# Kernel optimization log

Hardware: AMD Instinct MI355X
Metric: run time of the kernel (lower is better)

Reference implementation:

```python
import jax, jax.numpy as jnp
import numpy as np
from math import sqrt

N_USERS = 60000
N_ITEMS = 40000
D = 64
B = 3
LAYERS = 2
E = 600000
BATCH = 2048
N_NODES = (N_USERS + 1) + (N_ITEMS + 1)
REG_WEIGHT = 1e-3
BPR_GAMMA = 1e-10


def setup_inputs() -> dict:
    key = jax.random.key(0)
    k0, k1, k2, k3, k4 = jax.random.split(key, 5)
    user_emb = jax.random.normal(k0, (N_USERS + 1, D), jnp.float32) * 0.1
    item_emb = jax.random.normal(k1, (N_ITEMS + 1, D), jnp.float32) * 0.1
    W = jnp.ones((B,), jnp.float32)
    edge_users = jax.random.randint(k2, (B, E), 1, N_USERS + 1)
    edge_items = jax.random.randint(k3, (B, E), 1, N_ITEMS + 1)
    batch_data = jax.random.randint(k4, (BATCH, B, 3), 1, N_ITEMS + 1)
    return dict(user_emb=user_emb, item_emb=item_emb, W=W,
                edge_users=edge_users, edge_items=edge_items,
                batch_data=batch_data)


def _lightgcn(emb, eu, ei, layers):
    # bipartite undirected graph: users <-> items (items offset by N_USERS+1)
    it = ei + (N_USERS + 1)
    src = jnp.concatenate([eu, it])
    dst = jnp.concatenate([it, eu])
    deg = jax.ops.segment_sum(jnp.ones_like(src, jnp.float32), src, N_NODES)
    norm = jax.lax.rsqrt(jnp.maximum(deg[src], 1.0)) * jax.lax.rsqrt(jnp.maximum(deg[dst], 1.0))
    out = emb
    cur = emb
    for _ in range(layers):
        cur = jax.ops.segment_sum(cur[src] * norm[:, None], dst, N_NODES)
        out = out + cur
    return out / (layers + 1)


def _mutual_attention(f):
    # f: [N, B, D]
    S = jnp.einsum('nid,njd->nij', f, f)          # [N, B, B] pairwise scores
    last = S[:, B - 1:B, :]                        # [N, 1, B]
    proj = S[:, :B - 1, :]                         # [N, B-1, B]
    # (last * proj) * last / (last^2 + eps)   (dim-1 is size 1, sums/norms trivial)
    clear = (last * proj) * last / (last * last + 1e-12)   # [N, B-1, B]
    scores = jnp.sum(clear, axis=1, keepdims=True) + last   # [N, 1, B]
    all_scores = jnp.concatenate([clear, scores], axis=1)   # [N, B, B]
    att = jax.nn.softmax(all_scores / sqrt(D), axis=-1)
    return jnp.einsum('nij,njd->nid', att, f)


def reference(user_emb, item_emb, W, edge_users, edge_items, batch_data):
    total0 = jnp.concatenate([user_emb, item_emb], axis=0)   # [N_NODES, D]
    # global graph = union of all behaviors
    g_eu = edge_users.reshape(-1)
    g_ei = edge_items.reshape(-1)
    all_emb = _lightgcn(total0, g_eu, g_ei, LAYERS)
    # per-behavior propagation
    u_list, i_list = [], []
    for b in range(B):
        eb = _lightgcn(all_emb, edge_users[b], edge_items[b], LAYERS)
        u_list.append(eb[:N_USERS + 1])
        i_list.append(eb[N_USERS + 1:])
    all_user = jnp.stack(u_list, axis=1)   # [n_users+1, B, D]
    all_item = jnp.stack(i_list, axis=1)   # [n_items+1, B, D]
    all_user = _mutual_attention(all_user)
    # item behaviour degree: interactions per item per behavior
    ones = jnp.ones((E,), jnp.float32)
    ibd = jnp.stack([jax.ops.segment_sum(ones, edge_items[b], N_ITEMS + 1)
                     for b in range(B)], axis=1)   # [n_items+1, B]
    weight = ibd * W
    weight = weight / (jnp.sum(weight, axis=1, keepdims=True) + 1e-8)
    item_final = jnp.sum(all_item * weight[:, :, None], axis=1)   # [n_items+1, D]
    total_loss = jnp.float32(0.0)
    for b in range(B):
        users = batch_data[:, b, 0]
        items = batch_data[:, b, 1:3]
        uf = all_user[:, b][users][:, None, :]      # [batch, 1, D]
        itf = item_final[items]                      # [batch, 2, D]
        scores = jnp.sum(uf * itf, axis=2)           # [batch, 2]
        total_loss = total_loss - jnp.mean(
            jnp.log(BPR_GAMMA + jax.nn.sigmoid(scores[:, 0] - scores[:, 1])))
    emb_loss = (jnp.linalg.norm(user_emb) + jnp.linalg.norm(item_emb)) / (N_ITEMS + 1)
    return total_loss + REG_WEIGHT * emb_loss
```

## Files before the change

kernel.cpp:

```cpp
#include <hip/hip_runtime.h>
#include <hip/hip_bf16.h>
#include <math.h>

#define NUQ 60001
#define NIQ 40001
#define NNQ 100002
#define DQ  64
#define EQ  600000
#define BQ  3
#define BATCHQ 2048
#define ROWW 32
#define NSLOT (BATCHQ * BQ)
#define NPAD 100004
#define ADJB 1200000
#define BLK_ELE 2048
#define NBLK ((NNQ + BLK_ELE - 1) / BLK_ELE)
#define RANGE 392
#define NRANGE 256
#define NBINS (BQ * NRANGE)
#define NBLKA 256
#define EPB ((BQ * EQ + NBLKA - 1) / NBLKA)

__device__ __forceinline__ float wave_sum(float v) {
#pragma unroll
  for (int m = 32; m >= 1; m >>= 1) v += __shfl_xor(v, m, 64);
  return v;
}
__device__ __forceinline__ int wave_sum_i(int v) {
#pragma unroll
  for (int m = 32; m >= 1; m >>= 1) v += __shfl_xor(v, m, 64);
  return v;
}

__device__ __forceinline__ unsigned pack_bf2(float lo, float hi) {
  unsigned a = __float_as_uint(lo);
  unsigned b = __float_as_uint(hi);
  a = (a + 0x7FFFu + ((a >> 16) & 1u)) >> 16;
  b = (b + 0x7FFFu + ((b >> 16) & 1u)) >> 16;
  return a | (b << 16);
}
__device__ __forceinline__ float unpk_lo(unsigned u) { return __uint_as_float(u << 16); }
__device__ __forceinline__ float unpk_hi(unsigned u) { return __uint_as_float(u & 0xFFFF0000u); }

__device__ __forceinline__ void ntst_u32(unsigned* p, unsigned v) { __builtin_nontemporal_store(v, p); }
__device__ __forceinline__ void ntst_f32(float* p, float v) { __builtin_nontemporal_store(v, p); }
__device__ __forceinline__ unsigned ntld_u32(const unsigned* p) { return __builtin_nontemporal_load(p); }
__device__ __forceinline__ float ntld_f32(const float* p) { return __builtin_nontemporal_load(p); }

__global__ void zero_i_k(int* __restrict__ p, int n) {
  int tid = blockIdx.x * blockDim.x + threadIdx.x;
  int stride = gridDim.x * blockDim.x;
  for (int i = tid; i < n; i += stride) p[i] = 0;
}

__global__ void sumsq_k(const float* __restrict__ p, int n, float* __restrict__ acc) {
  int tid = blockIdx.x * blockDim.x + threadIdx.x;
  int stride = gridDim.x * blockDim.x;
  float s = 0.f;
  for (int i = tid; i < n; i += stride) { float v = p[i]; s += v * v; }
  s = wave_sum(s);
  __shared__ float ws[4];
  if ((threadIdx.x & 63) == 0) ws[threadIdx.x >> 6] = s;
  __syncthreads();
  if (threadIdx.x == 0) atomicAdd(acc, ws[0] + ws[1] + ws[2] + ws[3]);
}

__global__ void binc_k(const int* __restrict__ eu, const int* __restrict__ ei,
                       unsigned* __restrict__ counts) {
  __shared__ unsigned h[NBINS];
  for (int i = threadIdx.x; i < NBINS; i += 256) h[i] = 0u;
  __syncthreads();
  int base = blockIdx.x * EPB;
  int end = base + EPB;
  if (end > BQ * EQ) end = BQ * EQ;
  for (int idx = base + threadIdx.x; idx < end; idx += 256) {
    int b = idx / EQ;
    int u = eu[idx];
    int it = ei[idx] + NUQ;
    atomicAdd(&h[b * NRANGE + u / RANGE], 1u);
    atomicAdd(&h[b * NRANGE + it / RANGE], 1u);
  }
  __syncthreads();
  for (int i = threadIdx.x; i < NBINS; i += 256)
    counts[(size_t)blockIdx.x * NBINS + i] = h[i];
}

__global__ void binscan1_k(const unsigned* __restrict__ counts,
                           unsigned* __restrict__ offs, unsigned* __restrict__ bintot) {
  int bin = blockIdx.x;
  int t = threadIdx.x;
  int lane = t & 63, wid = t >> 6;
  unsigned v = counts[(size_t)t * NBINS + bin];
  unsigned incl = v;
#pragma unroll
  for (int off = 1; off < 64; off <<= 1) {
    unsigned x = __shfl_up(incl, off, 64);
    if (lane >= off) incl += x;
  }
  __shared__ unsigned wsum[4];
  if (lane == 63) wsum[wid] = incl;
  __syncthreads();
  if (t == 0) {
    unsigned s = 0;
#pragma unroll
    for (int w = 0; w < 4; ++w) { unsigned x = wsum[w]; wsum[w] = s; s += x; }
  }
  __syncthreads();
  unsigned excl = incl - v + wsum[wid];
  offs[(size_t)t * NBINS + bin] = excl;
  if (t == 255) bintot[bin] = excl + v;
}

__global__ void binscan2_k(const unsigned* __restrict__ bintot,
                           unsigned* __restrict__ binstart) {
  int t = threadIdx.x;
  int lane = t & 63, wid = t >> 6;
  unsigned c0 = bintot[t * 3 + 0], c1 = bintot[t * 3 + 1], c2 = bintot[t * 3 + 2];
  unsigned tsum = c0 + c1 + c2;
  unsigned incl = tsum;
#pragma unroll
  for (int off = 1; off < 64; off <<= 1) {
    unsigned x = __shfl_up(incl, off, 64);
    if (lane >= off) incl += x;
  }
  __shared__ unsigned wsum[4];
  if (lane == 63) wsum[wid] = incl;
  __syncthreads();
  if (t == 0) {
    unsigned s = 0;
#pragma unroll
    for (int w = 0; w < 4; ++w) { unsigned x = wsum[w]; wsum[w] = s; s += x; }
  }
  __syncthreads();
  unsigned run = incl - tsum + wsum[wid];
  binstart[t * 3 + 0] = run; run += c0;
  binstart[t * 3 + 1] = run; run += c1;
  binstart[t * 3 + 2] = run; run += c2;
  if (t == 255) binstart[NBINS] = run;
}

__global__ void binfill_k(const int* __restrict__ eu, const int* __restrict__ ei,
                          const unsigned* __restrict__ offs,
                          const unsigned* __restrict__ binstart,
                          unsigned* __restrict__ records) {
  __shared__ unsigned cur[NBINS];
  for (int i = threadIdx.x; i < NBINS; i += 256)
    cur[i] = binstart[i] + offs[(size_t)blockIdx.x * NBINS + i];
  __syncthreads();
  int base = blockIdx.x * EPB;
  int end = base + EPB;
  if (end > BQ * EQ) end = BQ * EQ;
  for (int idx = base + threadIdx.x; idx < end; idx += 256) {
    int b = idx / EQ;
    int u = eu[idx];
    int itl = ei[idx];
    int it = itl + NUQ;
    unsigned p = atomicAdd(&cur[b * NRANGE + u / RANGE], 1u);
    records[p] = ((unsigned)(u % RANGE) << 16) | (unsigned)itl;
    unsigned q = atomicAdd(&cur[b * NRANGE + it / RANGE], 1u);
    records[q] = ((unsigned)(it % RANGE) << 16) | (unsigned)u;
  }
}

__global__ void bindeg_k(const unsigned* __restrict__ records,
                         const unsigned* __restrict__ binstart,
                         int* __restrict__ degB) {
  int bin = blockIdx.x;
  int b = bin / NRANGE;
  int r0 = (bin % NRANGE) * RANGE;
  __shared__ int h[RANGE];
  for (int i = threadIdx.x; i < RANGE; i += 256) h[i] = 0;
  __syncthreads();
  unsigned rs = binstart[bin], re = binstart[bin + 1];
  for (unsigned j = rs + threadIdx.x; j < re; j += 256)
    atomicAdd(&h[records[j] >> 16], 1);
  __syncthreads();
  int nval = NNQ - r0;
  if (nval > RANGE) nval = RANGE;
  int* deg = degB + (size_t)b * NPAD;
  for (int i = threadIdx.x; i < nval; i += 256) deg[r0 + i] = h[i];
}

__global__ void scan_p1_k(const int* __restrict__ degB, int* __restrict__ partial) {
  int b = blockIdx.x / NBLK;
  int blk = blockIdx.x % NBLK;
  const int* deg = degB + (size_t)b * NPAD;
  int base = blk * BLK_ELE + threadIdx.x * 8;
  int s = 0;
#pragma unroll
  for (int i = 0; i < 8; ++i) { int idx = base + i; if (idx < NNQ) s += deg[idx]; }
  s = wave_sum_i(s);
  __shared__ int lds[4];
  int wid = threadIdx.x >> 6;
  if ((threadIdx.x & 63) == 0) lds[wid] = s;
  __syncthreads();
  if (threadIdx.x == 0) partial[b * NBLK + blk] = lds[0] + lds[1] + lds[2] + lds[3];
}

__global__ void scan_p2_k(int* __restrict__ partial, int* __restrict__ rowptrB) {
  int wid = threadIdx.x >> 6;
  int lane = threadIdx.x & 63;
  if (wid >= BQ) return;
  int v = (lane < NBLK) ? partial[wid * NBLK + lane] : 0;
  int orig = v;
#pragma unroll
  for (int off = 1; off < 64; off <<= 1) {
    int t = __shfl_up(v, off, 64);
    if (lane >= off) v += t;
  }
  if (lane < NBLK) partial[wid * NBLK + lane] = v - orig;
  if (lane == NBLK - 1) rowptrB[(size_t)wid * NPAD + NNQ] = v;
}

__global__ void scan_p3_k(const int* __restrict__ degB, const int* __restrict__ partial,
                          int* __restrict__ rowptrB, float* __restrict__ invsqB) {
  int b = blockIdx.x / NBLK;
  int blk = blockIdx.x % NBLK;
  const int* deg = degB + (size_t)b * NPAD;
  int* rowptr = rowptrB + (size_t)b * NPAD;
  float* invsq = invsqB + (size_t)b * NPAD;
  int base = blk * BLK_ELE + threadIdx.x * 8;
  int d[8];
  int tsum = 0;
#pragma unroll
  for (int i = 0; i < 8; ++i) {
    int idx = base + i;
    d[i] = (idx < NNQ) ? deg[idx] : 0;
    tsum += d[i];
  }
  int lane = threadIdx.x & 63;
  int wid = threadIdx.x >> 6;
  int incl = tsum;
#pragma unroll
  for (int off = 1; off < 64; off <<= 1) {
    int t = __shfl_up(incl, off, 64);
    if (lane >= off) incl += t;
  }
  int excl = incl - tsum;
  __shared__ int lds[4];
  if (lane == 63) lds[wid] = incl;
  __syncthreads();
  if (threadIdx.x == 0) {
    int s = 0;
#pragma unroll
    for (int w = 0; w < 4; ++w) { int t = lds[w]; lds[w] = s; s += t; }
  }
  __syncthreads();
  int run = excl + lds[wid] + partial[b * NBLK + blk];
#pragma unroll
  for (int i = 0; i < 8; ++i) {
    int idx = base + i;
    if (idx < NNQ) {
      rowptr[idx] = run;
      run += d[i];
      invsq[idx] = rsqrtf(fmaxf((float)d[i], 1.f));
    }
  }
}

__global__ void invsqg_k(const int* __restrict__ degB, float* __restrict__ invsqG) {
  int n = blockIdx.x * blockDim.x + threadIdx.x;
  if (n >= NNQ) return;
  int dg = degB[n] + degB[NPAD + n] + degB[2 * NPAD + n];
  invsqG[n] = rsqrtf(fmaxf((float)dg, 1.f));
}

__global__ void binscat_k(const unsigned* __restrict__ records,
                          const unsigned* __restrict__ binstart,
                          const int* __restrict__ rowptrB,
                          unsigned short* __restrict__ adjB) {
  int bin = blockIdx.x;
  int b = bin / NRANGE;
  int r0 = (bin % NRANGE) * RANGE;
  int nval = NNQ - r0;
  if (nval > RANGE) nval = RANGE;
  __shared__ int cur[RANGE];
  const int* rowptr = rowptrB + (size_t)b * NPAD;
  for (int i = threadIdx.x; i < nval; i += 256) cur[i] = rowptr[r0 + i];
  __syncthreads();
  unsigned rs = binstart[bin], re = binstart[bin + 1];
  unsigned short* adj = adjB + (size_t)b * ADJB;
  for (unsigned j = rs + threadIdx.x; j < re; j += 256) {
    unsigned rec = records[j];
    int dl = rec >> 16;
    int pos = atomicAdd(&cur[dl], 1);
    adj[pos] = (unsigned short)(rec & 0xFFFFu);
  }
}

__global__ void pack_emb_k(const float* __restrict__ ue, const float* __restrict__ ie,
                           unsigned* __restrict__ E0) {
  int idx = blockIdx.x * blockDim.x + threadIdx.x;
  if (idx >= NNQ * ROWW) return;
  int n = idx >> 5, k = idx & 31;
  const float* src = (n < NUQ) ? (ue + (size_t)n * DQ) : (ie + (size_t)(n - NUQ) * DQ);
  float a = src[2 * k], b = src[2 * k + 1];
  ntst_u32(&E0[idx], pack_bf2(a, b));
}

__device__ __forceinline__ void gather_w(const unsigned* __restrict__ S,
                                         const unsigned short* __restrict__ adj,
                                         const float* __restrict__ invsq,
                                         int start, int end, int offs,
                                         int lane, unsigned k4, int g,
                                         float& alo, float& ahi) {
  for (int j0 = start; j0 < end; j0 += 64) {
    int nloc = end - j0;
    if (nloc > 64) nloc = 64;
    unsigned boff = (unsigned)offs << 7;
    float w = 0.f;
    if (lane < nloc) {
      int a = (int)adj[j0 + lane] + offs;
      boff = (unsigned)a << 7;
      w = invsq[a];
    }
    for (int j = 0; j < nloc; j += 16) {
#pragma unroll
      for (int m = 0; m < 8; ++m) {
        int jj = j + 2 * m + g;
        unsigned bo = (unsigned)__shfl((int)boff, jj, 64) + k4;
        float ww = __shfl(w, jj, 64);
        unsigned dd = *(const unsigned*)((const char*)S + bo);
        alo += ww * unpk_lo(dd);
        ahi += ww * unpk_hi(dd);
      }
    }
  }
}

__device__ __forceinline__ void gather3w(const unsigned* __restrict__ S,
                                         const unsigned short* __restrict__ adjB,
                                         const float* __restrict__ wtab,
                                         int s0, int d0, int s1, int d1,
                                         int s2, int d2, int offs,
                                         int lane, unsigned k4, int g,
                                         float& alo, float& ahi) {
  int D = d0 + d1 + d2;
  int d01 = d0 + d1;
  for (int j0 = 0; j0 < D; j0 += 64) {
    int nloc = D - j0;
    if (nloc > 64) nloc = 64;
    unsigned boff = (unsigned)offs << 7;
    float w = 0.f;
    int l = j0 + lane;
    if (l < D) {
      int idx;
      if (l < d0)       idx = s0 + l;
      else if (l < d01) idx = ADJB + s1 + (l - d0);
      else              idx = 2 * ADJB + s2 + (l - d01);
      int a = (int)adjB[idx] + offs;
      boff = (unsigned)a << 7;
      w = wtab[a];
    }
    for (int j = 0; j < nloc; j += 16) {
#pragma unroll
      for (int m = 0; m < 8; ++m) {
        int jj = j + 2 * m + g;
        unsigned bo = (unsigned)__shfl((int)boff, jj, 64) + k4;
        float ww = __shfl(w, jj, 64);
        unsigned dd = *(const unsigned*)((const char*)S + bo);
        alo += ww * unpk_lo(dd);
        ahi += ww * unpk_hi(dd);
      }
    }
  }
}

__global__ void g_l1_k(const unsigned* __restrict__ E0, unsigned* __restrict__ T1,
                       const int* __restrict__ rowptrB, const unsigned short* __restrict__ adjB,
                       const float* __restrict__ invsqG) {
  int wid = (blockIdx.x * blockDim.x + threadIdx.x) >> 6;
  int lane = threadIdx.x & 63;
  if (wid >= NNQ) return;
  int k = lane & 31, g = lane >> 5;
  unsigned k4 = (unsigned)k << 2;
  int offs = (wid < NUQ) ? NUQ : 0;
  const int* rp0 = rowptrB;
  const int* rp1 = rowptrB + NPAD;
  const int* rp2 = rowptrB + 2 * (size_t)NPAD;
  int s0 = rp0[wid], d0 = rp0[wid + 1] - s0;
  int s1 = rp1[wid], d1 = rp1[wid + 1] - s1;
  int s2 = rp2[wid], d2 = rp2[wid + 1] - s2;
  float alo = 0.f, ahi = 0.f;
  gather3w(E0, adjB, invsqG, s0, d0, s1, d1, s2, d2, offs, lane, k4, g, alo, ahi);
  alo += __shfl_xor(alo, 32, 64);
  ahi += __shfl_xor(ahi, 32, 64);
  float s = invsqG[wid];
  if (lane < 32)
    ntst_u32(&T1[(size_t)wid * ROWW + k], pack_bf2(alo * s, ahi * s));
}

__global__ void g_l2c_k(const unsigned* __restrict__ E0, const unsigned* __restrict__ T1,
                        unsigned* __restrict__ C,
                        const int* __restrict__ rowptrB, const unsigned short* __restrict__ adjB,
                        const float* __restrict__ invsqG) {
  int wid = (blockIdx.x * blockDim.x + threadIdx.x) >> 6;
  int lane = threadIdx.x & 63;
  if (wid >= NNQ) return;
  int k = lane & 31, g = lane >> 5;
  unsigned k4 = (unsigned)k << 2;
  int offs = (wid < NUQ) ? NUQ : 0;
  const int* rp0 = rowptrB;
  const int* rp1 = rowptrB + NPAD;
  const int* rp2 = rowptrB + 2 * (size_t)NPAD;
  int s0 = rp0[wid], d0 = rp0[wid + 1] - s0;
  int s1 = rp1[wid], d1 = rp1[wid + 1] - s1;
  int s2 = rp2[wid], d2 = rp2[wid + 1] - s2;
  float alo = 0.f, ahi = 0.f;
  gather3w(T1, adjB, invsqG, s0, d0, s1, d1, s2, d2, offs, lane, k4, g, alo, ahi);
  alo += __shfl_xor(alo, 32, 64);
  ahi += __shfl_xor(ahi, 32, 64);
  if (lane < 32) {
    float s = invsqG[wid];
    unsigned e0 = E0[(size_t)wid * ROWW + k];
    unsigned t1 = T1[(size_t)wid * ROWW + k];
    float clo = (unpk_lo(e0) + unpk_lo(t1) + alo * s) * (1.f / 3.f);
    float chi = (unpk_hi(e0) + unpk_hi(t1) + ahi * s) * (1.f / 3.f);
    ntst_u32(&C[(size_t)wid * ROWW + k], pack_bf2(clo, chi));
  }
}

__global__ void b_l1_k(const unsigned* __restrict__ C, unsigned* __restrict__ T1B,
                       const int* __restrict__ rowptrB, const unsigned short* __restrict__ adjB,
                       const float* __restrict__ invsqB) {
  int wid = (blockIdx.x * blockDim.x + threadIdx.x) >> 6;
  int lane = threadIdx.x & 63;
  if (wid >= NNQ) return;
  int b = blockIdx.y;
  const int* rowptr = rowptrB + (size_t)b * NPAD;
  const float* iv = invsqB + (size_t)b * NPAD;
  int k = lane & 31, g = lane >> 5;
  unsigned k4 = (unsigned)k << 2;
  int offs = (wid < NUQ) ? NUQ : 0;
  float alo = 0.f, ahi = 0.f;
  gather_w(C, adjB + (size_t)b * ADJB, iv, rowptr[wid], rowptr[wid + 1], offs, lane, k4, g, alo, ahi);
  alo += __shfl_xor(alo, 32, 64);
  ahi += __shfl_xor(ahi, 32, 64);
  float s = iv[wid];
  if (lane < 32)
    ntst_u32(&T1B[(size_t)b * NNQ * ROWW + (size_t)wid * ROWW + k], pack_bf2(alo * s, ahi * s));
}

__global__ void slot_users_k(const unsigned* __restrict__ C, const unsigned* __restrict__ T1B,
                             const int* __restrict__ rowptrB, const unsigned short* __restrict__ adjB,
                             const float* __restrict__ invsqB,
                             const int* __restrict__ batch, float* __restrict__ UG) {
  int slot = (blockIdx.x * blockDim.x + threadIdx.x) >> 6;
  int lane = threadIdx.x & 63;
  if (slot >= NSLOT) return;
  int b = blockIdx.y;
  const int* rp = rowptrB + (size_t)b * NPAD;
  const float* iv = invsqB + (size_t)b * NPAD;
  const unsigned* T1 = T1B + (size_t)b * NNQ * ROWW;
  int u = batch[slot * 3 + 0];
  int k = lane & 31, g = lane >> 5;
  unsigned k4 = (unsigned)k << 2;
  float alo = 0.f, ahi = 0.f;
  gather_w(T1, adjB + (size_t)b * ADJB, iv, rp[u], rp[u + 1], NUQ, lane, k4, g, alo, ahi);
  alo += __shfl_xor(alo, 32, 64);
  ahi += __shfl_xor(ahi, 32, 64);
  float s = iv[u];
  unsigned c0 = C[(size_t)u * ROWW + k];
  unsigned t0 = T1[(size_t)u * ROWW + k];
  if (lane < 32) {
    size_t base = ((size_t)slot * BQ + b) * DQ;
    ntst_f32(&UG[base + 2 * k],     (unpk_lo(c0) + unpk_lo(t0) + alo * s) * (1.f / 3.f));
    ntst_f32(&UG[base + 2 * k + 1], (unpk_hi(c0) + unpk_hi(t0) + ahi * s) * (1.f / 3.f));
  }
}

__global__ void slot_items_k(const unsigned* __restrict__ C, const unsigned* __restrict__ T1B,
                             const int* __restrict__ rowptrB, const unsigned short* __restrict__ adjB,
                             const float* __restrict__ invsqB,
                             const int* __restrict__ batch, float* __restrict__ IG) {
  int islot = (blockIdx.x * blockDim.x + threadIdx.x) >> 6;
  int lane = threadIdx.x & 63;
  if (islot >= 2 * NSLOT) return;
  int b = blockIdx.y;
  const int* rp = rowptrB + (size_t)b * NPAD;
  const float* iv = invsqB + (size_t)b * NPAD;
  const unsigned* T1 = T1B + (size_t)b * NNQ * ROWW;
  int slot = islot >> 1;
  int c = (islot & 1) + 1;
  int n = batch[slot * 3 + c] + NUQ;
  int k = lane & 31, g = lane >> 5;
  unsigned k4 = (unsigned)k << 2;
  float alo = 0.f, ahi = 0.f;
  gather_w(T1, adjB + (size_t)b * ADJB, iv, rp[n], rp[n + 1], 0, lane, k4, g, alo, ahi);
  alo += __shfl_xor(alo, 32, 64);
  ahi += __shfl_xor(ahi, 32, 64);
  float s = iv[n];
  unsigned c0 = C[(size_t)n * ROWW + k];
  unsigned t0 = T1[(size_t)n * ROWW + k];
  if (lane < 32) {
    size_t base = ((size_t)islot * BQ + b) * DQ;
    ntst_f32(&IG[base + 2 * k],     (unpk_lo(c0) + unpk_lo(t0) + alo * s) * (1.f / 3.f));
    ntst_f32(&IG[base + 2 * k + 1], (unpk_hi(c0) + unpk_hi(t0) + ahi * s) * (1.f / 3.f));
  }
}

__global__ void epilogue_k(const float* __restrict__ UG, const float* __restrict__ IG,
                           const int* __restrict__ degB, const int* __restrict__ batch,
                           const float* __restrict__ W, float* __restrict__ acc) {
  int slot = (blockIdx.x * blockDim.x + threadIdx.x) >> 6;
  int lane = threadIdx.x & 63;
  float val = 0.f;
  if (slot < NSLOT) {
    int bb = slot % BQ;
    size_t base = (size_t)slot * (BQ * DQ) + lane;
    float a0 = ntld_f32(&UG[base]);
    float a1 = ntld_f32(&UG[base + 64]);
    float a2 = ntld_f32(&UG[base + 128]);
    float p00 = wave_sum(a0 * a0);
    float p01 = wave_sum(a0 * a1);
    float p02 = wave_sum(a0 * a2);
    float p11 = wave_sum(a1 * a1);
    float p12 = wave_sum(a1 * a2);
    float p22 = wave_sum(a2 * a2);
    float last[3] = {p02, p12, p22};
    float S0[3] = {p00, p01, p02};
    float S1[3] = {p01, p11, p12};
    float rows[3][3];
#pragma unroll
    for (int j = 0; j < 3; ++j) {
      float l = last[j];
      float f = l * l / (l * l + 1e-12f);
      float c0 = S0[j] * f;
      float c1 = S1[j] * f;
      rows[0][j] = c0;
      rows[1][j] = c1;
      rows[2][j] = c0 + c1 + l;
    }
    float x0 = rows[bb][0] * 0.125f, x1 = rows[bb][1] * 0.125f, x2 = rows[bb][2] * 0.125f;
    float m = fmaxf(x0, fmaxf(x1, x2));
    float e0 = expf(x0 - m), e1 = expf(x1 - m), e2 = expf(x2 - m);
    float inv = 1.f / (e0 + e1 + e2);
    float uf = (e0 * a0 + e1 * a1 + e2 * a2) * inv;
    float sco[2];
#pragma unroll
    for (int c = 0; c < 2; ++c) {
      int islot = slot * 2 + c;
      int node = batch[slot * 3 + 1 + c] + NUQ;
      float w0 = (float)degB[0 * NPAD + node] * W[0];
      float w1 = (float)degB[1 * NPAD + node] * W[1];
      float w2 = (float)degB[2 * NPAD + node] * W[2];
      float inv2 = 1.f / (w0 + w1 + w2 + 1e-8f);
      size_t rb = (size_t)islot * (BQ * DQ) + lane;
      float ifv = (ntld_f32(&IG[rb]) * w0 + ntld_f32(&IG[rb + 64]) * w1 +
                   ntld_f32(&IG[rb + 128]) * w2) * inv2;
      sco[c] = wave_sum(uf * ifv);
    }
    if (lane == 0) {
      float x = sco[0] - sco[1];
      float sg = 1.f / (1.f + expf(-x));
      val = -logf(1e-10f + sg) * (1.f / (float)BATCHQ);
    }
  }
  __shared__ float ws[4];
  if (lane == 0) ws[threadIdx.x >> 6] = val;
  __syncthreads();
  if (threadIdx.x == 0) atomicAdd(acc, ws[0] + ws[1] + ws[2] + ws[3]);
}

__global__ void finalize_k(const float* __restrict__ sc, unsigned int* __restrict__ out) {
  float total = sc[0] + 0.001f * (sqrtf(sc[1]) + sqrtf(sc[2])) / (float)NIQ;
  unsigned int bits = __float_as_uint(total);
  unsigned int lsb = (bits >> 16) & 1u;
  unsigned int rb = (bits + 0x7FFFu + lsb) >> 16;
  out[0] = (rb << 16) | rb;
}

extern "C" void kernel_launch(void* const* d_in, const int* in_sizes, int n_in,
                              void* d_out, int out_size, void* d_ws, size_t ws_size,
                              hipStream_t stream) {
  const float* ue = (const float*)d_in[0];
  const float* ie = (const float*)d_in[1];
  const float* W  = (const float*)d_in[2];
  const int* eu    = (const int*)d_in[3];
  const int* ei    = (const int*)d_in[4];
  const int* batch = (const int*)d_in[5];

  unsigned* E0  = (unsigned*)d_ws;
  unsigned* T1  = E0 + (size_t)NNQ * ROWW;
  unsigned* C   = T1 + (size_t)NNQ * ROWW;
  unsigned* T1B = C + (size_t)NNQ * ROWW;
  float* UG   = (float*)(T1B + (size_t)BQ * NNQ * ROWW);
  float* IG   = UG + (size_t)NSLOT * (BQ * DQ);
  unsigned short* adjB = (unsigned short*)(IG + (size_t)2 * NSLOT * (BQ * DQ));
  int* rowptrB= (int*)(adjB + (size_t)BQ * ADJB);
  int* degB   = rowptrB + 3 * NPAD;
  float* invsqB = (float*)(degB + 3 * NPAD);
  float* invsqG = invsqB + 3 * NPAD;
  unsigned* counts = (unsigned*)(invsqG + NPAD);
  unsigned* offs   = counts + (size_t)NBLKA * NBINS;
  unsigned* bintot = offs + (size_t)NBLKA * NBINS;
  unsigned* binstart = bintot + 1024;
  unsigned* records = binstart + 1024;
  int* partial  = (int*)(records + (size_t)2 * BQ * EQ);
  float* sc   = (float*)(partial + 256);

  zero_i_k<<<1, 64, 0, stream>>>((int*)sc, 8);
  sumsq_k<<<512, 256, 0, stream>>>(ue, NUQ * DQ, sc + 1);
  sumsq_k<<<512, 256, 0, stream>>>(ie, NIQ * DQ, sc + 2);

  binc_k<<<NBLKA, 256, 0, stream>>>(eu, ei, counts);
  binscan1_k<<<NBINS, 256, 0, stream>>>(counts, offs, bintot);
  binscan2_k<<<1, 256, 0, stream>>>(bintot, binstart);
  binfill_k<<<NBLKA, 256, 0, stream>>>(eu, ei, offs, binstart, records);
  bindeg_k<<<NBINS, 256, 0, stream>>>(records, binstart, degB);
  scan_p1_k<<<BQ * NBLK, 256, 0, stream>>>(degB, partial);
  scan_p2_k<<<1, 256, 0, stream>>>(partial, rowptrB);
  scan_p3_k<<<BQ * NBLK, 256, 0, stream>>>(degB, partial, rowptrB, invsqB);
  invsqg_k<<<(NNQ + 255) / 256, 256, 0, stream>>>(degB, invsqG);
  binscat_k<<<NBINS, 256, 0, stream>>>(records, binstart, rowptrB, adjB);

  pack_emb_k<<<(NNQ * ROWW + 255) / 256, 256, 0, stream>>>(ue, ie, E0);

  const int NODE_BLKS = (NNQ + 3) / 4;

  g_l1_k<<<NODE_BLKS, 256, 0, stream>>>(E0, T1, rowptrB, adjB, invsqG);
  g_l2c_k<<<NODE_BLKS, 256, 0, stream>>>(E0, T1, C, rowptrB, adjB, invsqG);

  b_l1_k<<<dim3(NODE_BLKS, 3), 256, 0, stream>>>(C, T1B, rowptrB, adjB, invsqB);

  slot_users_k<<<dim3((NSLOT + 3) / 4, 3), 256, 0, stream>>>(C, T1B, rowptrB, adjB, invsqB, batch, UG);
  slot_items_k<<<dim3((2 * NSLOT + 3) / 4, 3), 256, 0, stream>>>(C, T1B, rowptrB, adjB, invsqB, batch, IG);
  epilogue_k<<<(NSLOT + 3) / 4, 256, 0, stream>>>(UG, IG, degB, batch, W, sc);
  finalize_k<<<1, 1, 0, stream>>>(sc, (unsigned int*)d_out);
}
```

Before: 452.1 us.

## Map two graph nodes per wavefront using half-wave gathers

Every gather kernel (global layers, the per-behaviour layer, and the user and item slot kernels) now assigns one node to each 32-lane half-wave instead of one node to a full wave. Before, the two halves split a single node's neighbour list and then combined their partial sums with a cross-half shuffle. Now each half walks its own node's neighbours 8 at a time, which removes that reduction and the idle upper lanes at write-out, and halves the grid sizes. The slot kernels also write their results as 2-float vector nontemporal stores. The trade-off is that two nodes with different degrees now share one wave, so it runs until the longer neighbour list finishes, and each node's neighbours are processed more serially.

```diff
diff --git a/kernel.cpp b/kernel.cpp
--- a/kernel.cpp
+++ b/kernel.cpp
@@ -21,6 +21,8 @@
 #define NBLKA 256
 #define EPB ((BQ * EQ + NBLKA - 1) / NBLKA)
 
+typedef float f32x2 __attribute__((ext_vector_type(2)));
+
 __device__ __forceinline__ float wave_sum(float v) {
 #pragma unroll
   for (int m = 32; m >= 1; m >>= 1) v += __shfl_xor(v, m, 64);
@@ -44,7 +46,6 @@
 
 __device__ __forceinline__ void ntst_u32(unsigned* p, unsigned v) { __builtin_nontemporal_store(v, p); }
 __device__ __forceinline__ void ntst_f32(float* p, float v) { __builtin_nontemporal_store(v, p); }
-__device__ __forceinline__ unsigned ntld_u32(const unsigned* p) { return __builtin_nontemporal_load(p); }
 __device__ __forceinline__ float ntld_f32(const float* p) { return __builtin_nontemporal_load(p); }
 
 __global__ void zero_i_k(int* __restrict__ p, int n) {
@@ -298,26 +299,27 @@
   ntst_u32(&E0[idx], pack_bf2(a, b));
 }
 
-__device__ __forceinline__ void gather_w(const unsigned* __restrict__ S,
-                                         const unsigned short* __restrict__ adj,
-                                         const float* __restrict__ invsq,
-                                         int start, int end, int offs,
-                                         int lane, unsigned k4, int g,
-                                         float& alo, float& ahi) {
-  for (int j0 = start; j0 < end; j0 += 64) {
+
+__device__ __forceinline__ void gather_w32(const unsigned* __restrict__ S,
+                                           const unsigned short* __restrict__ adj,
+                                           const float* __restrict__ invsq,
+                                           int start, int end, int offs,
+                                           int l5, int g32, unsigned k4,
+                                           float& alo, float& ahi) {
+  for (int j0 = start; j0 < end; j0 += 32) {
     int nloc = end - j0;
-    if (nloc > 64) nloc = 64;
+    if (nloc > 32) nloc = 32;
     unsigned boff = (unsigned)offs << 7;
     float w = 0.f;
-    if (lane < nloc) {
-      int a = (int)adj[j0 + lane] + offs;
+    if (l5 < nloc) {
+      int a = (int)adj[j0 + l5] + offs;
       boff = (unsigned)a << 7;
       w = invsq[a];
     }
-    for (int j = 0; j < nloc; j += 16) {
+    for (int j = 0; j < nloc; j += 8) {
 #pragma unroll
       for (int m = 0; m < 8; ++m) {
-        int jj = j + 2 * m + g;
+        int jj = j + m + g32;
         unsigned bo = (unsigned)__shfl((int)boff, jj, 64) + k4;
         float ww = __shfl(w, jj, 64);
         unsigned dd = *(const unsigned*)((const char*)S + bo);
@@ -328,21 +330,21 @@
   }
 }
 
-__device__ __forceinline__ void gather3w(const unsigned* __restrict__ S,
-                                         const unsigned short* __restrict__ adjB,
-                                         const float* __restrict__ wtab,
-                                         int s0, int d0, int s1, int d1,
-                                         int s2, int d2, int offs,
-                                         int lane, unsigned k4, int g,
-                                         float& alo, float& ahi) {
+__device__ __forceinline__ void gather3w32(const unsigned* __restrict__ S,
+                                           const unsigned short* __restrict__ adjB,
+                                           const float* __restrict__ wtab,
+                                           int s0, int d0, int s1, int d1,
+                                           int s2, int d2, int offs,
+                                           int l5, int g32, unsigned k4,
+                                           float& alo, float& ahi) {
   int D = d0 + d1 + d2;
   int d01 = d0 + d1;
-  for (int j0 = 0; j0 < D; j0 += 64) {
+  for (int j0 = 0; j0 < D; j0 += 32) {
     int nloc = D - j0;
-    if (nloc > 64) nloc = 64;
+    if (nloc > 32) nloc = 32;
     unsigned boff = (unsigned)offs << 7;
     float w = 0.f;
-    int l = j0 + lane;
+    int l = j0 + l5;
     if (l < D) {
       int idx;
       if (l < d0)       idx = s0 + l;
@@ -352,10 +354,10 @@
       boff = (unsigned)a << 7;
       w = wtab[a];
     }
-    for (int j = 0; j < nloc; j += 16) {
+    for (int j = 0; j < nloc; j += 8) {
 #pragma unroll
       for (int m = 0; m < 8; ++m) {
-        int jj = j + 2 * m + g;
+        int jj = j + m + g32;
         unsigned bo = (unsigned)__shfl((int)boff, jj, 64) + k4;
         float ww = __shfl(w, jj, 64);
         unsigned dd = *(const unsigned*)((const char*)S + bo);
@@ -369,112 +371,106 @@
 __global__ void g_l1_k(const unsigned* __restrict__ E0, unsigned* __restrict__ T1,
                        const int* __restrict__ rowptrB, const unsigned short* __restrict__ adjB,
                        const float* __restrict__ invsqG) {
-  int wid = (blockIdx.x * blockDim.x + threadIdx.x) >> 6;
-  int lane = threadIdx.x & 63;
-  if (wid >= NNQ) return;
-  int k = lane & 31, g = lane >> 5;
-  unsigned k4 = (unsigned)k << 2;
-  int offs = (wid < NUQ) ? NUQ : 0;
-  const int* rp0 = rowptrB;
-  const int* rp1 = rowptrB + NPAD;
-  const int* rp2 = rowptrB + 2 * (size_t)NPAD;
-  int s0 = rp0[wid], d0 = rp0[wid + 1] - s0;
-  int s1 = rp1[wid], d1 = rp1[wid + 1] - s1;
-  int s2 = rp2[wid], d2 = rp2[wid + 1] - s2;
+  int wv = (blockIdx.x * blockDim.x + threadIdx.x) >> 6;
+  int lane = threadIdx.x & 63;
+  int g = lane >> 5;
+  int node = wv * 2 + g;
+  if (node >= NNQ) return;
+  int l5 = lane & 31, g32 = g << 5;
+  unsigned k4 = (unsigned)l5 << 2;
+  int offs = (node < NUQ) ? NUQ : 0;
+  int s0 = rowptrB[node], d0 = rowptrB[node + 1] - s0;
+  int s1 = rowptrB[NPAD + node], d1 = rowptrB[NPAD + node + 1] - s1;
+  int s2 = rowptrB[2 * NPAD + node], d2 = rowptrB[2 * NPAD + node + 1] - s2;
   float alo = 0.f, ahi = 0.f;
-  gather3w(E0, adjB, invsqG, s0, d0, s1, d1, s2, d2, offs, lane, k4, g, alo, ahi);
-  alo += __shfl_xor(alo, 32, 64);
-  ahi += __shfl_xor(ahi, 32, 64);
-  float s = invsqG[wid];
-  if (lane < 32)
-    ntst_u32(&T1[(size_t)wid * ROWW + k], pack_bf2(alo * s, ahi * s));
+  gather3w32(E0, adjB, invsqG, s0, d0, s1, d1, s2, d2, offs, l5, g32, k4, alo, ahi);
+  float s = invsqG[node];
+  ntst_u32(&T1[(size_t)node * ROWW + l5], pack_bf2(alo * s, ahi * s));
 }
 
 __global__ void g_l2c_k(const unsigned* __restrict__ E0, const unsigned* __restrict__ T1,
                         unsigned* __restrict__ C,
                         const int* __restrict__ rowptrB, const unsigned short* __restrict__ adjB,
                         const float* __restrict__ invsqG) {
-  int wid = (blockIdx.x * blockDim.x + threadIdx.x) >> 6;
-  int lane = threadIdx.x & 63;
-  if (wid >= NNQ) return;
-  int k = lane & 31, g = lane >> 5;
-  unsigned k4 = (unsigned)k << 2;
-  int offs = (wid < NUQ) ? NUQ : 0;
-  const int* rp0 = rowptrB;
-  const int* rp1 = rowptrB + NPAD;
-  const int* rp2 = rowptrB + 2 * (size_t)NPAD;
-  int s0 = rp0[wid], d0 = rp0[wid + 1] - s0;
-  int s1 = rp1[wid], d1 = rp1[wid + 1] - s1;
-  int s2 = rp2[wid], d2 = rp2[wid + 1] - s2;
+  int wv = (blockIdx.x * blockDim.x + threadIdx.x) >> 6;
+  int lane = threadIdx.x & 63;
+  int g = lane >> 5;
+  int node = wv * 2 + g;
+  if (node >= NNQ) return;
+  int l5 = lane & 31, g32 = g << 5;
+  unsigned k4 = (unsigned)l5 << 2;
+  int offs = (node < NUQ) ? NUQ : 0;
+  int s0 = rowptrB[node], d0 = rowptrB[node + 1] - s0;
+  int s1 = rowptrB[NPAD + node], d1 = rowptrB[NPAD + node + 1] - s1;
+  int s2 = rowptrB[2 * NPAD + node], d2 = rowptrB[2 * NPAD + node + 1] - s2;
   float alo = 0.f, ahi = 0.f;
-  gather3w(T1, adjB, invsqG, s0, d0, s1, d1, s2, d2, offs, lane, k4, g, alo, ahi);
-  alo += __shfl_xor(alo, 32, 64);
-  ahi += __shfl_xor(ahi, 32, 64);
-  if (lane < 32) {
-    float s = invsqG[wid];
-    unsigned e0 = E0[(size_t)wid * ROWW + k];
-    unsigned t1 = T1[(size_t)wid * ROWW + k];
-    float clo = (unpk_lo(e0) + unpk_lo(t1) + alo * s) * (1.f / 3.f);
-    float chi = (unpk_hi(e0) + unpk_hi(t1) + ahi * s) * (1.f / 3.f);
-    ntst_u32(&C[(size_t)wid * ROWW + k], pack_bf2(clo, chi));
-  }
+  gather3w32(T1, adjB, invsqG, s0, d0, s1, d1, s2, d2, offs, l5, g32, k4, alo, ahi);
+  float s = invsqG[node];
+  size_t rb = (size_t)node * ROWW + l5;
+  unsigned e0 = E0[rb];
+  unsigned t1 = T1[rb];
+  float clo = (unpk_lo(e0) + unpk_lo(t1) + alo * s) * (1.f / 3.f);
+  float chi = (unpk_hi(e0) + unpk_hi(t1) + ahi * s) * (1.f / 3.f);
+  ntst_u32(&C[rb], pack_bf2(clo, chi));
 }
 
 __global__ void b_l1_k(const unsigned* __restrict__ C, unsigned* __restrict__ T1B,
                        const int* __restrict__ rowptrB, const unsigned short* __restrict__ adjB,
                        const float* __restrict__ invsqB) {
-  int wid = (blockIdx.x * blockDim.x + threadIdx.x) >> 6;
-  int lane = threadIdx.x & 63;
-  if (wid >= NNQ) return;
+  int wv = (blockIdx.x * blockDim.x + threadIdx.x) >> 6;
+  int lane = threadIdx.x & 63;
+  int g = lane >> 5;
+  int node = wv * 2 + g;
+  if (node >= NNQ) return;
   int b = blockIdx.y;
   const int* rowptr = rowptrB + (size_t)b * NPAD;
   const float* iv = invsqB + (size_t)b * NPAD;
-  int k = lane & 31, g = lane >> 5;
-  unsigned k4 = (unsigned)k << 2;
-  int offs = (wid < NUQ) ? NUQ : 0;
+  int l5 = lane & 31, g32 = g << 5;
+  unsigned k4 = (unsigned)l5 << 2;
+  int offs = (node < NUQ) ? NUQ : 0;
   float alo = 0.f, ahi = 0.f;
-  gather_w(C, adjB + (size_t)b * ADJB, iv, rowptr[wid], rowptr[wid + 1], offs, lane, k4, g, alo, ahi);
-  alo += __shfl_xor(alo, 32, 64);
-  ahi += __shfl_xor(ahi, 32, 64);
-  float s = iv[wid];
-  if (lane < 32)
-    ntst_u32(&T1B[(size_t)b * NNQ * ROWW + (size_t)wid * ROWW + k], pack_bf2(alo * s, ahi * s));
+  gather_w32(C, adjB + (size_t)b * ADJB, iv, rowptr[node], rowptr[node + 1], offs, l5, g32, k4, alo, ahi);
+  float s = iv[node];
+  ntst_u32(&T1B[(size_t)b * NNQ * ROWW + (size_t)node * ROWW + l5], pack_bf2(alo * s, ahi * s));
 }
 
 __global__ void slot_users_k(const unsigned* __restrict__ C, const unsigned* __restrict__ T1B,
                              const int* __restrict__ rowptrB, const unsigned short* __restrict__ adjB,
                              const float* __restrict__ invsqB,
                              const int* __restrict__ batch, float* __restrict__ UG) {
-  int slot = (blockIdx.x * blockDim.x + threadIdx.x) >> 6;
-  int lane = threadIdx.x & 63;
+  int wv = (blockIdx.x * blockDim.x + threadIdx.x) >> 6;
+  int lane = threadIdx.x & 63;
+  int g = lane >> 5;
+  int slot = wv * 2 + g;
   if (slot >= NSLOT) return;
   int b = blockIdx.y;
   const int* rp = rowptrB + (size_t)b * NPAD;
   const float* iv = invsqB + (size_t)b * NPAD;
   const unsigned* T1 = T1B + (size_t)b * NNQ * ROWW;
   int u = batch[slot * 3 + 0];
-  int k = lane & 31, g = lane >> 5;
-  unsigned k4 = (unsigned)k << 2;
+  int l5 = lane & 31, g32 = g << 5;
+  unsigned k4 = (unsigned)l5 << 2;
   float alo = 0.f, ahi = 0.f;
-  gather_w(T1, adjB + (size_t)b * ADJB, iv, rp[u], rp[u + 1], NUQ, lane, k4, g, alo, ahi);
-  alo += __shfl_xor(alo, 32, 64);
-  ahi += __shfl_xor(ahi, 32, 64);
+  gather_w32(T1, adjB + (size_t)b * ADJB, iv, rp[u], rp[u + 1], NUQ, l5, g32, k4, alo, ahi);
   float s = iv[u];
-  unsigned c0 = C[(size_t)u * ROWW + k];
-  unsigned t0 = T1[(size_t)u * ROWW + k];
-  if (lane < 32) {
-    size_t base = ((size_t)slot * BQ + b) * DQ;
-    ntst_f32(&UG[base + 2 * k],     (unpk_lo(c0) + unpk_lo(t0) + alo * s) * (1.f / 3.f));
-    ntst_f32(&UG[base + 2 * k + 1], (unpk_hi(c0) + unpk_hi(t0) + ahi * s) * (1.f / 3.f));
-  }
+  size_t rb = (size_t)u * ROWW + l5;
+  unsigned c0 = C[rb];
+  unsigned t0 = T1[rb];
+  size_t base = ((size_t)slot * BQ + b) * DQ + 2 * l5;
+  f32x2 o;
+  o.x = (unpk_lo(c0) + unpk_lo(t0) + alo * s) * (1.f / 3.f);
+  o.y = (unpk_hi(c0) + unpk_hi(t0) + ahi * s) * (1.f / 3.f);
+  __builtin_nontemporal_store(o, (f32x2*)&UG[base]);
 }
 
 __global__ void slot_items_k(const unsigned* __restrict__ C, const unsigned* __restrict__ T1B,
                              const int* __restrict__ rowptrB, const unsigned short* __restrict__ adjB,
                              const float* __restrict__ invsqB,
                              const int* __restrict__ batch, float* __restrict__ IG) {
-  int islot = (blockIdx.x * blockDim.x + threadIdx.x) >> 6;
-  int lane = threadIdx.x & 63;
+  int wv = (blockIdx.x * blockDim.x + threadIdx.x) >> 6;
+  int lane = threadIdx.x & 63;
+  int g = lane >> 5;
+  int islot = wv * 2 + g;
   if (islot >= 2 * NSLOT) return;
   int b = blockIdx.y;
   const int* rp = rowptrB + (size_t)b * NPAD;
@@ -483,20 +479,19 @@
   int slot = islot >> 1;
   int c = (islot & 1) + 1;
   int n = batch[slot * 3 + c] + NUQ;
-  int k = lane & 31, g = lane >> 5;
-  unsigned k4 = (unsigned)k << 2;
+  int l5 = lane & 31, g32 = g << 5;
+  unsigned k4 = (unsigned)l5 << 2;
   float alo = 0.f, ahi = 0.f;
-  gather_w(T1, adjB + (size_t)b * ADJB, iv, rp[n], rp[n + 1], 0, lane, k4, g, alo, ahi);
-  alo += __shfl_xor(alo, 32, 64);
-  ahi += __shfl_xor(ahi, 32, 64);
+  gather_w32(T1, adjB + (size_t)b * ADJB, iv, rp[n], rp[n + 1], 0, l5, g32, k4, alo, ahi);
   float s = iv[n];
-  unsigned c0 = C[(size_t)n * ROWW + k];
-  unsigned t0 = T1[(size_t)n * ROWW + k];
-  if (lane < 32) {
-    size_t base = ((size_t)islot * BQ + b) * DQ;
-    ntst_f32(&IG[base + 2 * k],     (unpk_lo(c0) + unpk_lo(t0) + alo * s) * (1.f / 3.f));
-    ntst_f32(&IG[base + 2 * k + 1], (unpk_hi(c0) + unpk_hi(t0) + ahi * s) * (1.f / 3.f));
-  }
+  size_t rb = (size_t)n * ROWW + l5;
+  unsigned c0 = C[rb];
+  unsigned t0 = T1[rb];
+  size_t base = ((size_t)islot * BQ + b) * DQ + 2 * l5;
+  f32x2 o;
+  o.x = (unpk_lo(c0) + unpk_lo(t0) + alo * s) * (1.f / 3.f);
+  o.y = (unpk_hi(c0) + unpk_hi(t0) + ahi * s) * (1.f / 3.f);
+  __builtin_nontemporal_store(o, (f32x2*)&IG[base]);
 }
 
 __global__ void epilogue_k(const float* __restrict__ UG, const float* __restrict__ IG,
@@ -616,15 +611,15 @@
 
   pack_emb_k<<<(NNQ * ROWW + 255) / 256, 256, 0, stream>>>(ue, ie, E0);
 
-  const int NODE_BLKS = (NNQ + 3) / 4;
-
-  g_l1_k<<<NODE_BLKS, 256, 0, stream>>>(E0, T1, rowptrB, adjB, invsqG);
-  g_l2c_k<<<NODE_BLKS, 256, 0, stream>>>(E0, T1, C, rowptrB, adjB, invsqG);
-
-  b_l1_k<<<dim3(NODE_BLKS, 3), 256, 0, stream>>>(C, T1B, rowptrB, adjB, invsqB);
-
-  slot_users_k<<<dim3((NSLOT + 3) / 4, 3), 256, 0, stream>>>(C, T1B, rowptrB, adjB, invsqB, batch, UG);
-  slot_items_k<<<dim3((2 * NSLOT + 3) / 4, 3), 256, 0, stream>>>(C, T1B, rowptrB, adjB, invsqB, batch, IG);
+  const int NODE_BLKS2 = (NNQ / 2 + 4) / 4;
+
+  g_l1_k<<<NODE_BLKS2, 256, 0, stream>>>(E0, T1, rowptrB, adjB, invsqG);
+  g_l2c_k<<<NODE_BLKS2, 256, 0, stream>>>(E0, T1, C, rowptrB, adjB, invsqG);
+
+  b_l1_k<<<dim3(NODE_BLKS2, 3), 256, 0, stream>>>(C, T1B, rowptrB, adjB, invsqB);
+
+  slot_users_k<<<dim3(NSLOT / 8, 3), 256, 0, stream>>>(C, T1B, rowptrB, adjB, invsqB, batch, UG);
+  slot_items_k<<<dim3(2 * NSLOT / 8, 3), 256, 0, stream>>>(C, T1B, rowptrB, adjB, invsqB, batch, IG);
   epilogue_k<<<(NSLOT + 3) / 4, 256, 0, stream>>>(UG, IG, degB, batch, W, sc);
   finalize_k<<<1, 1, 0, stream>>>(sc, (unsigned int*)d_out);
 }
```

Measured after the change: 415.8 us. 1.09x faster.
